# Kernel tuning notes

Measured on AMD Instinct MI355X. Metric: run time of the kernel, lower is better.

The kernel has to match this reference:

```python
import jax, jax.numpy as jnp
import numpy as np


def _bilinear_sample(fea, x, y):
    # fea: [B,C,H,W]; x,y: [B,D,HW] pixel coords. grid_sample bilinear, zeros padding, align_corners=True
    B, C, H, W = fea.shape
    x0 = jnp.floor(x)
    y0 = jnp.floor(y)
    wx1 = x - x0
    wy1 = y - y0
    flat = fea.reshape(B, C, H * W)

    def corner(xi, yi, w):
        valid = (xi >= 0) & (xi <= W - 1) & (yi >= 0) & (yi <= H - 1)
        idx = jnp.clip(yi, 0, H - 1).astype(jnp.int32) * W + jnp.clip(xi, 0, W - 1).astype(jnp.int32)
        v = jnp.take_along_axis(flat[:, :, None, :], idx[:, None, :, :], axis=3)  # [B,C,D,HW]
        return v * (w * valid)[:, None]

    return (corner(x0, y0, (1 - wx1) * (1 - wy1)) + corner(x0 + 1, y0, wx1 * (1 - wy1))
            + corner(x0, y0 + 1, (1 - wx1) * wy1) + corner(x0 + 1, y0 + 1, wx1 * wy1))


def _build_proj(p):
    # p: [B,2,4,4] -> 4x4 with top 3x4 = K @ [R|t]
    top = jnp.einsum('bij,bjk->bik', p[:, 1, :3, :3], p[:, 0, :3, :4])
    return p[:, 0].at[:, :3, :4].set(top)


def _forward(depth_values, features, proj_matrices, depth_interval, view_weights, CostNum):
    V = features.shape[0]
    ref_fea = features[0]
    B, C, H, W = ref_fea.shape
    # inverse-depth range sampling (per-pixel, CasMVSNet-style)
    inv_d = 1.0 / depth_values[:, 0]                      # [B,H,W]
    itv = depth_interval[:, 0]                            # [B,H,W]
    low = inv_d - (CostNum / 2.0) * itv
    step = (CostNum * itv) / (CostNum - 1)                # (high-low)/(D-1)
    samp = low[:, None] + jnp.arange(CostNum, dtype=inv_d.dtype)[None, :, None, None] * step[:, None]
    depth = (1.0 / samp).reshape(B, CostNum, H * W)       # back to metric depth [B,D,HW]

    ref_inv = jnp.linalg.inv(_build_proj(proj_matrices[:, 0]))
    ys, xs = jnp.meshgrid(jnp.arange(H, dtype=inv_d.dtype), jnp.arange(W, dtype=inv_d.dtype), indexing='ij')
    xyz = jnp.stack([xs.ravel(), ys.ravel(), jnp.ones(H * W, dtype=inv_d.dtype)], 0)  # [3,HW]

    vol = jnp.zeros((B, 1, CostNum, H, W), inv_d.dtype)
    wsum = jnp.full((B, 1, 1, H, W), 1e-5, inv_d.dtype)
    for i in range(1, V):
        proj = jnp.einsum('bij,bjk->bik', _build_proj(proj_matrices[:, i]), ref_inv)
        rot_xyz = jnp.einsum('bij,jn->bin', proj[:, :3, :3], xyz)                     # [B,3,HW]
        pxyz = rot_xyz[:, :, None, :] * depth[:, None] + proj[:, :3, 3][:, :, None, None]
        gx = pxyz[:, 0] / pxyz[:, 2]
        gy = pxyz[:, 1] / pxyz[:, 2]
        warped = _bilinear_sample(features[i], gx, gy).reshape(B, C, CostNum, H, W)
        wv = (warped * ref_fea[:, :, None]).mean(axis=1, keepdims=True)               # [B,1,D,H,W]
        vw = view_weights[:, i - 1][:, None, None]                                    # [B,1,1,H,W]
        vol = vol + wv * vw
        wsum = wsum + vw
    sim = vol / wsum
    # torch broadcasts [B,1,D,H,W] into the [B,C,D,H,W] buffer -> all C channels equal
    return jnp.broadcast_to(sim, (B, C, CostNum, H, W)).reshape(B, C * CostNum, H, W)


def setup_inputs():
    key = jax.random.key(0)
    ks = jax.random.split(key, 4)
    V, B, C, H, W = 5, 2, 32, 256, 320
    features = jax.random.normal(ks[0], (V, B, C, H, W), jnp.float32)
    depth_values = jax.random.uniform(ks[1], (B, 1, H, W), jnp.float32, minval=0.5, maxval=2.0)
    depth_interval = jax.random.uniform(ks[2], (B, 1, H, W), jnp.float32, minval=0.01, maxval=0.03)
    view_weights = jax.random.uniform(ks[3], (B, V - 1, H, W), jnp.float32, minval=0.1, maxval=1.0)
    K = np.array([[300.0, 0.0, W / 2.0], [0.0, 300.0, H / 2.0], [0.0, 0.0, 1.0]], np.float32)
    proj = np.zeros((B, V, 2, 4, 4), np.float32)
    for v in range(V):
        E = np.eye(4, dtype=np.float32)
        E[0, 3] = 0.1 * v  # camera baseline along x
        proj[:, v, 0] = E
        proj[:, v, 1] = np.eye(4, dtype=np.float32)
        proj[:, v, 1, :3, :3] = K
    return {"depth_values": depth_values, "features": features, "proj_matrices": jnp.asarray(proj),
            "depth_interval": depth_interval, "depth_max": 100, "depth_min": 1, "CostNum": 4,
            "view_weights": view_weights}


def reference(depth_values, features, proj_matrices, depth_interval, depth_max, depth_min, CostNum, view_weights):
    # depth_max/depth_min are unused in the per-pixel sampling path of the original helper
    return _forward(depth_values, features, proj_matrices, depth_interval, view_weights, CostNum)
```

## Files before the change

kernel.cpp:

```cpp
#include <hip/hip_runtime.h>

static constexpr int V  = 5;
static constexpr int B  = 2;
static constexpr int C  = 32;
static constexpr int H  = 256;
static constexpr int W  = 320;
static constexpr int CN = 4;
static constexpr int HW = H * W;
static constexpr int CG = 8;
static constexpr int NG = 4;
static constexpr int XT = W / 64;
static constexpr int NBLK = XT * H * B;

static constexpr size_t PARAMS_OFF = 0;

typedef float f32x2 __attribute__((ext_vector_type(2)));
typedef float f32x4 __attribute__((ext_vector_type(4)));

__device__ __forceinline__ f32x2 ld2(const float* p) {
    f32x2 v;
    __builtin_memcpy(&v, p, sizeof(f32x2));
    return v;
}

__global__ void setup_proj_kernel(const float* __restrict__ pm, float* __restrict__ params) {
    int b = threadIdx.x;
    if (b >= B) return;

    float M[V][16];
    for (int v = 0; v < V; ++v) {
        const float* E  = pm + ((size_t)(b * V + v) * 2 + 0) * 16;
        const float* Km = pm + ((size_t)(b * V + v) * 2 + 1) * 16;
        for (int r = 0; r < 3; ++r)
            for (int c = 0; c < 4; ++c) {
                float s = 0.f;
                for (int k = 0; k < 3; ++k) s += Km[r * 4 + k] * E[k * 4 + c];
                M[v][r * 4 + c] = s;
            }
        for (int c = 0; c < 4; ++c) M[v][12 + c] = E[12 + c];
    }

    float A[9], bb[3];
    for (int r = 0; r < 3; ++r) {
        for (int c = 0; c < 3; ++c) A[r * 3 + c] = M[0][r * 4 + c];
        bb[r] = M[0][r * 4 + 3];
    }
    float det = A[0] * (A[4] * A[8] - A[5] * A[7])
              - A[1] * (A[3] * A[8] - A[5] * A[6])
              + A[2] * (A[3] * A[7] - A[4] * A[6]);
    float id = 1.f / det;
    float Ai[9];
    Ai[0] = (A[4] * A[8] - A[5] * A[7]) * id;
    Ai[1] = (A[2] * A[7] - A[1] * A[8]) * id;
    Ai[2] = (A[1] * A[5] - A[2] * A[4]) * id;
    Ai[3] = (A[5] * A[6] - A[3] * A[8]) * id;
    Ai[4] = (A[0] * A[8] - A[2] * A[6]) * id;
    Ai[5] = (A[2] * A[3] - A[0] * A[5]) * id;
    Ai[6] = (A[3] * A[7] - A[4] * A[6]) * id;
    Ai[7] = (A[1] * A[6] - A[0] * A[7]) * id;
    Ai[8] = (A[0] * A[4] - A[1] * A[3]) * id;
    float bi[3];
    for (int r = 0; r < 3; ++r)
        bi[r] = -(Ai[r * 3 + 0] * bb[0] + Ai[r * 3 + 1] * bb[1] + Ai[r * 3 + 2] * bb[2]);

    float Minv[16];
    for (int r = 0; r < 3; ++r) {
        for (int c = 0; c < 3; ++c) Minv[r * 4 + c] = Ai[r * 3 + c];
        Minv[r * 4 + 3] = bi[r];
    }
    Minv[12] = 0.f; Minv[13] = 0.f; Minv[14] = 0.f; Minv[15] = 1.f;

    for (int v = 1; v < V; ++v) {
        float* dst = params + (size_t)(b * (V - 1) + (v - 1)) * 12;
        for (int r = 0; r < 3; ++r)
            for (int c = 0; c < 4; ++c) {
                float s = 0.f;
                for (int k = 0; k < 4; ++k) s += M[v][r * 4 + k] * Minv[k * 4 + c];
                dst[r * 4 + c] = s;
            }
    }
}

__global__ __launch_bounds__(256) void fused_kernel(
    const float* __restrict__ depth_values,
    const float* __restrict__ features,
    const float* __restrict__ depth_interval,
    const float* __restrict__ view_weights,
    const float* __restrict__ params,
    float* __restrict__ out)
{
    const int tid = threadIdx.x;
    const int p   = tid & 63;
    const int g   = tid >> 6;

    const int d   = blockIdx.x;
    const int u   = d >> 3;
    const int r8  = d & 7;
    const int xt  = u % XT;
    const int rid = r8 * 64 + u / XT;
    const int y   = rid & (H - 1);
    const int b   = rid >> 8;

    const int x   = xt * 64 + p;
    const int pix = y * W + x;

    __shared__ float sp4[48];
    __shared__ float stage[NG][1920];
    float* const sredp = &stage[0][0];
    float* const simp  = &stage[0][1024];

    if (tid < 48) sp4[tid] = params[(size_t)b * 48 + tid];
    __syncthreads();

    const float invd = 1.f / depth_values[(size_t)b * HW + pix];
    const float itv  = depth_interval[(size_t)b * HW + pix];
    const float low  = invd - (CN * 0.5f) * itv;
    const float step = (CN * itv) / (float)(CN - 1);
    float dep[CN];
#pragma unroll
    for (int k = 0; k < CN; ++k) dep[k] = 1.f / (low + (float)k * step);

    float vws[V - 1];
#pragma unroll
    for (int i = 0; i < V - 1; ++i)
        vws[i] = view_weights[((size_t)b * (V - 1) + i) * HW + pix];
    float wsum = 1e-5f;
#pragma unroll
    for (int i = 0; i < V - 1; ++i) wsum += vws[i];

    const float* refp = features + ((size_t)b * C + g * CG) * HW + pix;
    float rf[CG];
#pragma unroll
    for (int c = 0; c < CG; ++c) rf[c] = __builtin_nontemporal_load(refp + (size_t)c * HW);

    int soff[8];
#pragma unroll
    for (int it = 0; it < 8; ++it) {
        const int slot = it * 64 + p;
        const int f    = slot * 4;
        const int chl  = (f >= 960) ? 1 : 0;
        const int rem  = f - chl * 960;
        const int j    = rem / 320;
        const int col  = rem - j * 320;
        const int row  = min(max(y - 1 + j, 0), H - 1);
        soff[it] = chl * HW + row * W + col;
    }

    const float* srcgv[V - 1];
#pragma unroll
    for (int i = 0; i < V - 1; ++i)
        srcgv[i] = features + ((size_t)((i + 1) * B + b) * C + g * CG) * HW;

    const float fx = (float)x, fy = (float)y;
    float volsum[CN] = {0.f, 0.f, 0.f, 0.f};

    f32x4 R[8];
#pragma unroll
    for (int it = 0; it < 8; ++it)
        if (it < 7 || p < 32) R[it] = *(const f32x4*)(srcgv[0] + soff[it]);

    for (int iv = 0; iv < V - 1; ++iv) {
        const float* spv = &sp4[iv * 12];
        const float rx = spv[0] * fx + spv[1] * fy + spv[2];
        const float ry = spv[4] * fx + spv[5] * fy + spv[6];
        const float rz = spv[8] * fx + spv[9] * fy + spv[10];
        const float tx = spv[3], ty = spv[7], tz = spv[11];

        const float scale = vws[iv] * (1.f / (float)C);

        int   bx_[CN], y0_[CN];
        float wA0[CN], wB0[CN], wA1[CN], wB1[CN];
#pragma unroll
        for (int k = 0; k < CN; ++k) {
            const float dd = dep[k];
            const float px = rx * dd + tx;
            const float py = ry * dd + ty;
            const float pz = rz * dd + tz;
            const float iz = 1.f / pz;
            const float gx = px * iz;
            const float gy = py * iz;

            const float x0f = floorf(gx), y0f = floorf(gy);
            const float wx1 = gx - x0f, wy1 = gy - y0f;
            const float wx0 = 1.f - wx1, wy0 = 1.f - wy1;
            const int x0 = (int)x0f, y0 = (int)y0f;
            const int x1 = x0 + 1, y1 = y0 + 1;

            const bool vx0 = (x0 >= 0) && (x0 <= W - 1);
            const bool vx1 = (x1 >= 0) && (x1 <= W - 1);
            const bool vy0 = (y0 >= 0) && (y0 <= H - 1);
            const bool vy1 = (y1 >= 0) && (y1 <= H - 1);

            const int bx = min(max(x0, 0), W - 2);
            const int s  = x0 - bx;

            const float w00 = wx0 * wy0 * ((vx0 && vy0) ? scale : 0.f);
            const float w10 = wx1 * wy0 * ((vx1 && vy0) ? scale : 0.f);
            const float w01 = wx0 * wy1 * ((vx0 && vy1) ? scale : 0.f);
            const float w11 = wx1 * wy1 * ((vx1 && vy1) ? scale : 0.f);

            wA0[k] = (s == 0) ? w00 : ((s == -1) ? w10 : 0.f);
            wB0[k] = (s == 0) ? w10 : ((s == 1) ? w00 : 0.f);
            wA1[k] = (s == 0) ? w01 : ((s == -1) ? w11 : 0.f);
            wB1[k] = (s == 0) ? w11 : ((s == 1) ? w01 : 0.f);

            bx_[k] = bx;
            y0_[k] = y0;
        }

        bool okrow = true;
#pragma unroll
        for (int k = 0; k < CN; ++k)
            okrow = okrow && (y0_[k] >= y - 1) && (y0_[k] <= y);

        if (__all(okrow)) {
            int o0[CN];
#pragma unroll
            for (int k = 0; k < CN; ++k)
                o0[k] = (y0_[k] - y + 1) * 320 + bx_[k];

#pragma unroll
            for (int ph = 0; ph < 4; ++ph) {
#pragma unroll
                for (int it = 0; it < 8; ++it)
                    if (it < 7 || p < 32)
                        *(f32x4*)&stage[g][(it * 64 + p) * 4] = R[it];

                if (ph < 3) {
                    const float* nsrc = srcgv[iv] + (size_t)(2 * (ph + 1)) * HW;
#pragma unroll
                    for (int it = 0; it < 8; ++it)
                        if (it < 7 || p < 32) R[it] = *(const f32x4*)(nsrc + soff[it]);
                } else if (iv < V - 2) {
                    const float* nsrc = srcgv[iv + 1];
#pragma unroll
                    for (int it = 0; it < 8; ++it)
                        if (it < 7 || p < 32) R[it] = *(const f32x4*)(nsrc + soff[it]);
                }

#pragma unroll
                for (int c2 = 0; c2 < 2; ++c2) {
                    const float rfc = rf[2 * ph + c2];
                    const float* L = &stage[g][c2 * 960];
#pragma unroll
                    for (int k = 0; k < CN; ++k) {
                        const f32x2 a  = ld2(L + o0[k]);
                        const f32x2 b2 = ld2(L + o0[k] + 320);
                        float t = wA0[k] * a.x;
                        t = fmaf(wB0[k], a.y, t);
                        t = fmaf(wA1[k], b2.x, t);
                        t = fmaf(wB1[k], b2.y, t);
                        volsum[k] = fmaf(rfc, t, volsum[k]);
                    }
                }
            }
        } else {
            int ib0[CN], ib1[CN];
#pragma unroll
            for (int k = 0; k < CN; ++k) {
                const int cy0 = min(max(y0_[k],     0), H - 1);
                const int cy1 = min(max(y0_[k] + 1, 0), H - 1);
                ib0[k] = cy0 * W + bx_[k];
                ib1[k] = cy1 * W + bx_[k];
            }
            const float* srcg = srcgv[iv];
#pragma unroll 1
            for (int c = 0; c < CG; ++c) {
                const float* fc  = srcg + (size_t)c * HW;
                const float  rfc = rf[c];
#pragma unroll 1
                for (int k = 0; k < CN; ++k) {
                    const f32x2 a   = ld2(fc + ib0[k]);
                    const f32x2 bb2 = ld2(fc + ib1[k]);
                    float t = wA0[k] * a.x;
                    t = fmaf(wB0[k], a.y, t);
                    t = fmaf(wA1[k], bb2.x, t);
                    t = fmaf(wB1[k], bb2.y, t);
                    volsum[k] = fmaf(rfc, t, volsum[k]);
                }
            }
            if (iv < V - 2) {
#pragma unroll
                for (int it = 0; it < 8; ++it)
                    if (it < 7 || p < 32) R[it] = *(const f32x4*)(srcgv[iv + 1] + soff[it]);
            }
        }
    }

    __syncthreads();
#pragma unroll
    for (int k = 0; k < CN; ++k) sredp[(g * CN + k) * 64 + p] = volsum[k];
    __syncthreads();

    {
        const int k = g;
        const float s = sredp[(0 * CN + k) * 64 + p] + sredp[(1 * CN + k) * 64 + p]
                      + sredp[(2 * CN + k) * 64 + p] + sredp[(3 * CN + k) * 64 + p];
        simp[k * 64 + p] = s * (1.f / wsum);
    }
    __syncthreads();

    {
        const int quad = tid & 15;
        const int pc   = tid >> 4;
        float* op = out + (size_t)b * C * CN * HW + y * W + xt * 64 + quad * 4;
#pragma unroll
        for (int j = 0; j < 8; ++j) {
            const int plane = pc * 8 + j;
            const int k     = plane & 3;
            const f32x4 v   = *(const f32x4*)&simp[k * 64 + quad * 4];
            *(f32x4*)(op + (size_t)plane * HW) = v;
        }
    }
}

extern "C" void kernel_launch(void* const* d_in, const int* in_sizes, int n_in,
                              void* d_out, int out_size, void* d_ws, size_t ws_size,
                              hipStream_t stream) {
    const float* depth_values   = (const float*)d_in[0];
    const float* features       = (const float*)d_in[1];
    const float* proj_matrices  = (const float*)d_in[2];
    const float* depth_interval = (const float*)d_in[3];
    const float* view_weights   = (const float*)d_in[7];
    float* out    = (float*)d_out;
    float* params = (float*)d_ws + PARAMS_OFF;

    setup_proj_kernel<<<1, B, 0, stream>>>(proj_matrices, params);

    fused_kernel<<<NBLK, 256, 0, stream>>>(depth_values, features, depth_interval,
                                           view_weights, params, out);
}
```

Baseline: 326.6 us.

## Stage one channel at a time to shrink LDS and registers for occupancy

The per-wave shared-memory staging buffer now holds one channel of three rows instead of two channels. The register prefetch buffer is halved to match, source pointers are advanced by a stride instead of kept in an array, and launch bounds request 5 blocks per CU. The intent is to cut LDS and VGPR use so more waves can be resident and hide gather latency. In exchange there are twice as many smaller load and store rounds per view, which leaves less memory-level parallelism per wave. The fallback path also recomputes the row index per depth and indexes weight arrays dynamically, which may spill them to scratch.

```diff
diff --git a/kernel.cpp b/kernel.cpp
--- a/kernel.cpp
+++ b/kernel.cpp
@@ -81,7 +81,7 @@
     }
 }
 
-__global__ __launch_bounds__(256) void fused_kernel(
+__global__ __launch_bounds__(256, 5) void fused_kernel(
     const float* __restrict__ depth_values,
     const float* __restrict__ features,
     const float* __restrict__ depth_interval,
@@ -105,9 +105,9 @@
     const int pix = y * W + x;
 
     __shared__ float sp4[48];
-    __shared__ float stage[NG][1920];
+    __shared__ float stage[NG][960];
     float* const sredp = &stage[0][0];
-    float* const simp  = &stage[0][1024];
+    float* const simp  = &stage[0][0] + 1024;
 
     if (tid < 48) sp4[tid] = params[(size_t)b * 48 + tid];
     __syncthreads();
@@ -133,33 +133,28 @@
 #pragma unroll
     for (int c = 0; c < CG; ++c) rf[c] = __builtin_nontemporal_load(refp + (size_t)c * HW);
 
-    int soff[8];
-#pragma unroll
-    for (int it = 0; it < 8; ++it) {
-        const int slot = it * 64 + p;
-        const int f    = slot * 4;
-        const int chl  = (f >= 960) ? 1 : 0;
-        const int rem  = f - chl * 960;
-        const int j    = rem / 320;
-        const int col  = rem - j * 320;
-        const int row  = min(max(y - 1 + j, 0), H - 1);
-        soff[it] = chl * HW + row * W + col;
-    }
-
-    const float* srcgv[V - 1];
-#pragma unroll
-    for (int i = 0; i < V - 1; ++i)
-        srcgv[i] = features + ((size_t)((i + 1) * B + b) * C + g * CG) * HW;
+    int soff[4];
+#pragma unroll
+    for (int it = 0; it < 4; ++it) {
+        const int f   = (it * 64 + p) * 4;
+        const int j   = (f >= 640) ? 2 : ((f >= 320) ? 1 : 0);
+        const int col = f - j * 320;
+        const int row = min(max(y - 1 + j, 0), H - 1);
+        soff[it] = row * W + col;
+    }
+
+    const size_t VSTRIDE = (size_t)B * C * HW;
+    const float* src = features + ((size_t)(B + b) * C + g * CG) * HW;
 
     const float fx = (float)x, fy = (float)y;
     float volsum[CN] = {0.f, 0.f, 0.f, 0.f};
 
-    f32x4 R[8];
-#pragma unroll
-    for (int it = 0; it < 8; ++it)
-        if (it < 7 || p < 32) R[it] = *(const f32x4*)(srcgv[0] + soff[it]);
-
-    for (int iv = 0; iv < V - 1; ++iv) {
+    f32x4 R[4];
+#pragma unroll
+    for (int it = 0; it < 4; ++it)
+        if (it < 3 || p < 48) R[it] = *(const f32x4*)(src + soff[it]);
+
+    for (int iv = 0; iv < V - 1; ++iv, src += VSTRIDE) {
         const float* spv = &sp4[iv * 12];
         const float rx = spv[0] * fx + spv[1] * fy + spv[2];
         const float ry = spv[4] * fx + spv[5] * fy + spv[6];
@@ -168,7 +163,7 @@
 
         const float scale = vws[iv] * (1.f / (float)C);
 
-        int   bx_[CN], y0_[CN];
+        int   o0[CN];
         float wA0[CN], wB0[CN], wA1[CN], wB1[CN];
 #pragma unroll
         for (int k = 0; k < CN; ++k) {
@@ -204,85 +199,71 @@
             wA1[k] = (s == 0) ? w01 : ((s == -1) ? w11 : 0.f);
             wB1[k] = (s == 0) ? w11 : ((s == 1) ? w01 : 0.f);
 
-            bx_[k] = bx;
-            y0_[k] = y0;
+            o0[k] = (y0 - y + 1) * 320 + bx;
         }
 
         bool okrow = true;
 #pragma unroll
         for (int k = 0; k < CN; ++k)
-            okrow = okrow && (y0_[k] >= y - 1) && (y0_[k] <= y);
+            okrow = okrow && ((unsigned)o0[k] <= 638u);
 
         if (__all(okrow)) {
-            int o0[CN];
-#pragma unroll
-            for (int k = 0; k < CN; ++k)
-                o0[k] = (y0_[k] - y + 1) * 320 + bx_[k];
-
-#pragma unroll
-            for (int ph = 0; ph < 4; ++ph) {
-#pragma unroll
-                for (int it = 0; it < 8; ++it)
-                    if (it < 7 || p < 32)
+#pragma unroll
+            for (int ch = 0; ch < CG; ++ch) {
+#pragma unroll
+                for (int it = 0; it < 4; ++it)
+                    if (it < 3 || p < 48)
                         *(f32x4*)&stage[g][(it * 64 + p) * 4] = R[it];
 
-                if (ph < 3) {
-                    const float* nsrc = srcgv[iv] + (size_t)(2 * (ph + 1)) * HW;
-#pragma unroll
-                    for (int it = 0; it < 8; ++it)
-                        if (it < 7 || p < 32) R[it] = *(const f32x4*)(nsrc + soff[it]);
-                } else if (iv < V - 2) {
-                    const float* nsrc = srcgv[iv + 1];
-#pragma unroll
-                    for (int it = 0; it < 8; ++it)
-                        if (it < 7 || p < 32) R[it] = *(const f32x4*)(nsrc + soff[it]);
+                const bool more = (ch < CG - 1) || (iv < V - 2);
+                if (more) {
+                    const float* nsrc = (ch < CG - 1) ? src + (size_t)(ch + 1) * HW
+                                                      : src + VSTRIDE;
+#pragma unroll
+                    for (int it = 0; it < 4; ++it)
+                        if (it < 3 || p < 48) R[it] = *(const f32x4*)(nsrc + soff[it]);
                 }
 
-#pragma unroll
-                for (int c2 = 0; c2 < 2; ++c2) {
-                    const float rfc = rf[2 * ph + c2];
-                    const float* L = &stage[g][c2 * 960];
-#pragma unroll
-                    for (int k = 0; k < CN; ++k) {
-                        const f32x2 a  = ld2(L + o0[k]);
-                        const f32x2 b2 = ld2(L + o0[k] + 320);
-                        float t = wA0[k] * a.x;
-                        t = fmaf(wB0[k], a.y, t);
-                        t = fmaf(wA1[k], b2.x, t);
-                        t = fmaf(wB1[k], b2.y, t);
-                        volsum[k] = fmaf(rfc, t, volsum[k]);
-                    }
+                const float rfc = rf[ch];
+                const float* L = &stage[g][0];
+#pragma unroll
+                for (int k = 0; k < CN; ++k) {
+                    const f32x2 a  = ld2(L + o0[k]);
+                    const f32x2 b2 = ld2(L + o0[k] + 320);
+                    float t = wA0[k] * a.x;
+                    t = fmaf(wB0[k], a.y, t);
+                    t = fmaf(wA1[k], b2.x, t);
+                    t = fmaf(wB1[k], b2.y, t);
+                    volsum[k] = fmaf(rfc, t, volsum[k]);
                 }
             }
         } else {
-            int ib0[CN], ib1[CN];
-#pragma unroll
+#pragma unroll 1
             for (int k = 0; k < CN; ++k) {
-                const int cy0 = min(max(y0_[k],     0), H - 1);
-                const int cy1 = min(max(y0_[k] + 1, 0), H - 1);
-                ib0[k] = cy0 * W + bx_[k];
-                ib1[k] = cy1 * W + bx_[k];
-            }
-            const float* srcg = srcgv[iv];
+                const float dd = dep[k];
+                const float gy = (ry * dd + ty) / (rz * dd + tz);
+                const int   y0 = (int)floorf(gy);
+                const int  cy0 = min(max(y0,     0), H - 1);
+                const int  cy1 = min(max(y0 + 1, 0), H - 1);
+                const int   bx = o0[k] - (y0 - y + 1) * 320;
+                const int  ib0 = cy0 * W + bx;
+                const int  ib1 = cy1 * W + bx;
 #pragma unroll 1
-            for (int c = 0; c < CG; ++c) {
-                const float* fc  = srcg + (size_t)c * HW;
-                const float  rfc = rf[c];
-#pragma unroll 1
-                for (int k = 0; k < CN; ++k) {
-                    const f32x2 a   = ld2(fc + ib0[k]);
-                    const f32x2 bb2 = ld2(fc + ib1[k]);
+                for (int c = 0; c < CG; ++c) {
+                    const float* fc  = src + (size_t)c * HW;
+                    const f32x2 a   = ld2(fc + ib0);
+                    const f32x2 bb2 = ld2(fc + ib1);
                     float t = wA0[k] * a.x;
                     t = fmaf(wB0[k], a.y, t);
                     t = fmaf(wA1[k], bb2.x, t);
                     t = fmaf(wB1[k], bb2.y, t);
-                    volsum[k] = fmaf(rfc, t, volsum[k]);
+                    volsum[k] = fmaf(rf[c], t, volsum[k]);
                 }
             }
             if (iv < V - 2) {
 #pragma unroll
-                for (int it = 0; it < 8; ++it)
-                    if (it < 7 || p < 32) R[it] = *(const f32x4*)(srcgv[iv + 1] + soff[it]);
+                for (int it = 0; it < 4; ++it)
+                    if (it < 3 || p < 48) R[it] = *(const f32x4*)(src + VSTRIDE + soff[it]);
             }
         }
     }
```

Result: slower. 902.9 us (+176.4%).
